# Optimization experiments

Hardware: AMD Instinct MI355X
Metric: run time of the kernel (lower is better)

## Reference

```python
import jax, jax.numpy as jnp
import numpy as np

N_QUBITS = 8
N_LAYERS = 2
DIM = 2 ** N_QUBITS  # 256
SBERT_DIM = 768
BATCH = 65536

# PauliZ sign table: wire 0 is the most-significant bit (PennyLane convention).
_idx = np.arange(DIM)
_bits = (_idx[None, :] >> (N_QUBITS - 1 - np.arange(N_QUBITS))[:, None]) & 1
_SIGNS = (1.0 - 2.0 * _bits).astype(np.float32)  # [N_QUBITS, DIM]


def _apply_ry(state, theta, q):
    """Apply RY(theta) on qubit q. state: [B, 2]*8; theta: [B] or scalar.
    RY is real, so the statevector stays real-valued throughout."""
    c = jnp.cos(theta * 0.5)
    s = jnp.sin(theta * 0.5)
    if jnp.ndim(c) == 1:  # per-sample angles -> broadcast over qubit axes
        bshape = (c.shape[0],) + (1,) * (N_QUBITS - 1)
        c = c.reshape(bshape)
        s = s.reshape(bshape)
    s0 = jnp.take(state, 0, axis=q + 1)
    s1 = jnp.take(state, 1, axis=q + 1)
    return jnp.stack([c * s0 - s * s1, s * s0 + c * s1], axis=q + 1)


def _apply_cnot(state, ctrl, tgt):
    """CNOT with control=ctrl, target=tgt (tgt > ctrl here)."""
    a0 = jnp.take(state, 0, axis=ctrl + 1)
    a1 = jnp.take(state, 1, axis=ctrl + 1)
    # target axis index after removing the control axis
    t_ax = tgt if tgt > ctrl else tgt + 1
    a1 = jnp.flip(a1, axis=t_ax)  # flip target amplitude when control=1
    return jnp.stack([a0, a1], axis=ctrl + 1)


def _circuit(angles, weights):
    """Batched 8-qubit statevector simulation. angles: [B, 8]; weights: [2, 8].
    Returns <Z_i> for each wire: [B, 8]."""
    B = angles.shape[0]
    state = jnp.zeros((B, DIM), angles.dtype).at[:, 0].set(1.0)
    state = state.reshape((B,) + (2,) * N_QUBITS)
    for q in range(N_QUBITS):
        state = _apply_ry(state, angles[:, q], q)
    for layer in range(N_LAYERS):
        for q in range(N_QUBITS):
            state = _apply_ry(state, weights[layer, q], q)
        for q in range(N_QUBITS - 1):
            state = _apply_cnot(state, q, q + 1)
    probs = (state * state).reshape(B, DIM)
    return probs @ jnp.asarray(_SIGNS, dtype=probs.dtype).T  # [B, 8]


def setup_inputs() -> dict:
    key = jax.random.key(0)
    k_x, k_w, k_q = jax.random.split(key, 3)
    x = jax.random.normal(k_x, (BATCH, SBERT_DIM), dtype=jnp.float32)
    W_proj = jax.random.normal(k_w, (N_QUBITS, SBERT_DIM), dtype=jnp.float32) * (1.0 / np.sqrt(SBERT_DIM))
    scale = jnp.asarray(np.pi / 2.0, dtype=jnp.float32)
    weights = 0.01 * jax.random.normal(k_q, (N_LAYERS, N_QUBITS), dtype=jnp.float32)
    return {"x": x, "W_proj": W_proj, "scale": scale, "weights": weights}


def reference(x, W_proj, scale, weights):
    h = jnp.tanh(x @ W_proj.T) * scale  # [B, 8]
    return _circuit(h, weights).astype(jnp.float32)
```

## Files before the change

kernel.cpp:

```cpp
#include <hip/hip_runtime.h>


__device__ __forceinline__ float fast_tanh(float v) {
    float e = __expf(2.0f * v);
    return 1.0f - 2.0f / (e + 1.0f);
}

__device__ __forceinline__ void fwd_step(float (&L)[2][3], float A, float B,
                                         float c2, float cs) {
    float u[2][3];
    #pragma unroll
    for (int b = 0; b < 2; ++b) {
        const float v0 = L[b][0], v1 = L[b][1], v2 = L[b][2];
        const float d  = v0 - v2;
        const float B2 = B + B;
        u[b][0] = fmaf(A, d, fmaf(B2, v1, v2));
        u[b][1] = fmaf(B, v0 + v2, v1);
        u[b][2] = fmaf(-A, d, fmaf(B2, v1, v0));
    }
    const float d0 = u[0][0] - u[1][0];
    L[0][0] = fmaf(c2, d0, u[1][0]);
    L[1][0] = fmaf(-c2, d0, u[0][0]);
    const float m = cs * (u[1][1] - u[0][1]);
    L[0][1] = m;  L[1][1] = -m;
    const float d2 = u[1][2] - u[0][2];
    L[0][2] = fmaf(c2, d2, u[0][2]);
    L[1][2] = fmaf(-c2, d2, u[1][2]);
}

__global__ __launch_bounds__(256, 3)
void pqc_kernel(const float* __restrict__ x,
                const float* __restrict__ Wp,
                const float* __restrict__ scalep,
                const float* __restrict__ wts,
                float* __restrict__ out)
{
    const int tid  = threadIdx.x;
    const int lane = tid & 63;
    const int wave = tid >> 6;
    const int b0   = blockIdx.x * 64;

    const int s4  = lane >> 4;
    const int c16 = lane & 15;

    const int rbase = b0 + wave * 16;
    float acc[4][8];
    #pragma unroll
    for (int p = 0; p < 4; ++p)
        #pragma unroll
        for (int q = 0; q < 8; ++q) acc[p][q] = 0.0f;

    #pragma unroll 2
    for (int j = 0; j < 12; ++j) {
        const int col4 = j * 16 + c16;
        float4 wv[8];
        #pragma unroll
        for (int q = 0; q < 8; ++q)
            wv[q] = *reinterpret_cast<const float4*>(Wp + q * 768 + col4 * 4);
        #pragma unroll
        for (int p = 0; p < 4; ++p) {
            const float4 xv = *reinterpret_cast<const float4*>(
                x + (size_t)(rbase + p * 4 + s4) * 768 + col4 * 4);
            #pragma unroll
            for (int q = 0; q < 8; ++q) {
                acc[p][q] = fmaf(xv.x, wv[q].x, acc[p][q]);
                acc[p][q] = fmaf(xv.y, wv[q].y, acc[p][q]);
                acc[p][q] = fmaf(xv.z, wv[q].z, acc[p][q]);
                acc[p][q] = fmaf(xv.w, wv[q].w, acc[p][q]);
            }
        }
    }
    #pragma unroll
    for (int m = 1; m <= 8; m <<= 1)
        #pragma unroll
        for (int p = 0; p < 4; ++p)
            #pragma unroll
            for (int q = 0; q < 8; ++q)
                acc[p][q] += __shfl_xor(acc[p][q], m, 64);


    const float scl = scalep[0];
    const int  k    = lane & 7;
    const bool i0   = (lane & 8) != 0;

    float c2q[8], csq[8];
    #pragma unroll
    for (int q = 0; q < 8; ++q) {
        float sw, cw;
        __sincosf(0.5f * wts[8 + q], &sw, &cw);
        c2q[q] = cw * cw;  csq[q] = cw * sw;
    }

    #pragma unroll
    for (int pass = 0; pass < 2; ++pass) {
        float Aq[8], Bq[8];
        #pragma unroll
        for (int q = 0; q < 8; ++q) {
            const float hq = i0 ? acc[pass * 2 + 1][q] : acc[pass * 2][q];
            float ang = fast_tanh(hq) * scl + wts[q];
            float s, c;
            __sincosf(0.5f * ang, &s, &c);
            Aq[q] = c * c;  Bq[q] = c * s;
        }

        float L[2][3] = {{1.f, 0.f, 0.f}, {0.f, 0.f, 0.f}};
        #pragma unroll
        for (int q = 0; q < 8; ++q) {
            fwd_step(L, Aq[q], Bq[q], c2q[q], csq[q]);
            const float sgn = (q == k) ? -1.f : 1.f;
            L[1][0] *= sgn;  L[1][1] *= sgn;  L[1][2] *= sgn;
        }
        const float zv = (L[0][0] + 2.f * L[0][1] + L[0][2])
                       + (L[1][0] + 2.f * L[1][1] + L[1][2]);

        const int p = pass * 2 + (i0 ? 1 : 0);
        out[(size_t)(rbase + p * 4 + s4) * 8 + k] = zv;
    }
}

extern "C" void kernel_launch(void* const* d_in, const int* in_sizes, int n_in,
                              void* d_out, int out_size, void* d_ws, size_t ws_size,
                              hipStream_t stream) {
    const float* x   = (const float*)d_in[0];
    const float* W   = (const float*)d_in[1];
    const float* sc  = (const float*)d_in[2];
    const float* wt  = (const float*)d_in[3];
    float* o         = (float*)d_out;

    const int batch  = in_sizes[0] / 768;
    const int blocks = batch / 64;
    pqc_kernel<<<dim3(blocks), dim3(256), 0, stream>>>(x, W, sc, wt, o);
}
```

Before: 45.56 us.

## Split K across wave pairs, stage W in LDS, one output per thread

Each block now handles 32 rows instead of 64. Two waves split the 768-wide reduction in halves and their partial sums are combined through shared memory. W_proj is staged into LDS once per block, and the circuit epilogue is remapped so each of the 256 threads computes one (row, wire) output in a single pass with a coalesced store. The occupancy hint moves to waves_per_eu(5). These changes add more parallelism for the memory-bound projection and remove the two-pass epilogue, at the cost of two block barriers, 24KB of LDS per block and twice as many blocks each reloading W.

New measurement: 54.08 us. 1.19x slower.

```diff
diff --git a/kernel.cpp b/kernel.cpp
--- a/kernel.cpp
+++ b/kernel.cpp
@@ -28,35 +28,52 @@
     L[1][2] = fmaf(-c2, d2, u[1][2]);
 }
 
-__global__ __launch_bounds__(256, 3)
+__global__ __launch_bounds__(256)
+__attribute__((amdgpu_waves_per_eu(5)))
 void pqc_kernel(const float* __restrict__ x,
                 const float* __restrict__ Wp,
                 const float* __restrict__ scalep,
                 const float* __restrict__ wts,
                 float* __restrict__ out)
 {
+    __shared__ float Wl[6144];
+    __shared__ float hb[2][2][16][8];
+
     const int tid  = threadIdx.x;
     const int lane = tid & 63;
     const int wave = tid >> 6;
-    const int b0   = blockIdx.x * 64;
+    const int g    = wave >> 1;
+    const int kh   = wave & 1;
+    const int b0   = blockIdx.x * 32;
+    const int rbase = b0 + g * 16;
 
     const int s4  = lane >> 4;
     const int c16 = lane & 15;
 
-    const int rbase = b0 + wave * 16;
+    {
+        const float4* Wv4 = reinterpret_cast<const float4*>(Wp);
+        float4*       Lv4 = reinterpret_cast<float4*>(Wl);
+        #pragma unroll
+        for (int k = 0; k < 6; ++k)
+            Lv4[tid + k * 256] = Wv4[tid + k * 256];
+    }
+    __syncthreads();
+
     float acc[4][8];
     #pragma unroll
     for (int p = 0; p < 4; ++p)
         #pragma unroll
         for (int q = 0; q < 8; ++q) acc[p][q] = 0.0f;
 
+    const int colbase = kh * 96 + c16;
+
     #pragma unroll 2
-    for (int j = 0; j < 12; ++j) {
-        const int col4 = j * 16 + c16;
+    for (int j = 0; j < 6; ++j) {
+        const int col4 = colbase + j * 16;
         float4 wv[8];
         #pragma unroll
         for (int q = 0; q < 8; ++q)
-            wv[q] = *reinterpret_cast<const float4*>(Wp + q * 768 + col4 * 4);
+            wv[q] = *reinterpret_cast<const float4*>(Wl + q * 768 + col4 * 4);
         #pragma unroll
         for (int p = 0; p < 4; ++p) {
             const float4 xv = *reinterpret_cast<const float4*>(
@@ -70,6 +87,7 @@
             }
         }
     }
+
     #pragma unroll
     for (int m = 1; m <= 8; m <<= 1)
         #pragma unroll
@@ -78,44 +96,43 @@
             for (int q = 0; q < 8; ++q)
                 acc[p][q] += __shfl_xor(acc[p][q], m, 64);
 
+    if (c16 == 0) {
+        #pragma unroll
+        for (int p = 0; p < 4; ++p)
+            #pragma unroll
+            for (int q = 0; q < 8; ++q)
+                hb[g][kh][p * 4 + s4][q] = acc[p][q];
+    }
+    __syncthreads();
 
+    const int s5 = tid >> 3;
+    const int k  = tid & 7;
     const float scl = scalep[0];
-    const int  k    = lane & 7;
-    const bool i0   = (lane & 8) != 0;
 
-    float c2q[8], csq[8];
+    float Aq[8], Bq[8], c2q[8], csq[8];
     #pragma unroll
     for (int q = 0; q < 8; ++q) {
+        const float hq = hb[s5 >> 4][0][s5 & 15][q] + hb[s5 >> 4][1][s5 & 15][q];
+        float ang = fast_tanh(hq) * scl + wts[q];
+        float s, c;
+        __sincosf(0.5f * ang, &s, &c);
+        Aq[q] = c * c;  Bq[q] = c * s;
         float sw, cw;
         __sincosf(0.5f * wts[8 + q], &sw, &cw);
         c2q[q] = cw * cw;  csq[q] = cw * sw;
     }
 
+    float L[2][3] = {{1.f, 0.f, 0.f}, {0.f, 0.f, 0.f}};
     #pragma unroll
-    for (int pass = 0; pass < 2; ++pass) {
-        float Aq[8], Bq[8];
-        #pragma unroll
-        for (int q = 0; q < 8; ++q) {
-            const float hq = i0 ? acc[pass * 2 + 1][q] : acc[pass * 2][q];
-            float ang = fast_tanh(hq) * scl + wts[q];
-            float s, c;
-            __sincosf(0.5f * ang, &s, &c);
-            Aq[q] = c * c;  Bq[q] = c * s;
-        }
+    for (int q = 0; q < 8; ++q) {
+        fwd_step(L, Aq[q], Bq[q], c2q[q], csq[q]);
+        const float sgn = (q == k) ? -1.f : 1.f;
+        L[1][0] *= sgn;  L[1][1] *= sgn;  L[1][2] *= sgn;
+    }
+    const float zv = (L[0][0] + 2.f * L[0][1] + L[0][2])
+                   + (L[1][0] + 2.f * L[1][1] + L[1][2]);
 
-        float L[2][3] = {{1.f, 0.f, 0.f}, {0.f, 0.f, 0.f}};
-        #pragma unroll
-        for (int q = 0; q < 8; ++q) {
-            fwd_step(L, Aq[q], Bq[q], c2q[q], csq[q]);
-            const float sgn = (q == k) ? -1.f : 1.f;
-            L[1][0] *= sgn;  L[1][1] *= sgn;  L[1][2] *= sgn;
-        }
-        const float zv = (L[0][0] + 2.f * L[0][1] + L[0][2])
-                       + (L[1][0] + 2.f * L[1][1] + L[1][2]);
-
-        const int p = pass * 2 + (i0 ? 1 : 0);
-        out[(size_t)(rbase + p * 4 + s4) * 8 + k] = zv;
-    }
+    out[(size_t)b0 * 8 + tid] = zv;
 }
 
 extern "C" void kernel_launch(void* const* d_in, const int* in_sizes, int n_in,
@@ -128,6 +145,6 @@
     float* o         = (float*)d_out;
 
     const int batch  = in_sizes[0] / 768;
-    const int blocks = batch / 64;
+    const int blocks = batch / 32;
     pqc_kernel<<<dim3(blocks), dim3(256), 0, stream>>>(x, W, sc, wt, o);
 }
```
